# Kernel tuning notes

Hardware: AMD Instinct MI355X
Metric: run time of the kernel (lower is better)

Reference implementation:

```python
import jax, jax.numpy as jnp
import numpy as np

N = 10000
E = 320000


def setup_inputs() -> dict:
    key = jax.random.key(0)
    ks = jax.random.split(key, 10)
    return {
        "x": jax.random.normal(ks[0], (N, 384), dtype=jnp.float32),
        "edge_index": jax.random.randint(ks[1], (2, E), 0, N, dtype=jnp.int64)
        if jax.config.jax_enable_x64 else jax.random.randint(ks[1], (2, E), 0, N, dtype=jnp.int32),
        "W1": jax.random.normal(ks[2], (256, 384), dtype=jnp.float32) * 0.05,
        "b1": jax.random.normal(ks[3], (256,), dtype=jnp.float32) * 0.05,
        "W2": jax.random.normal(ks[4], (128, 256), dtype=jnp.float32) * 0.05,
        "b2": jax.random.normal(ks[5], (128,), dtype=jnp.float32) * 0.05,
        "Wa1": jax.random.normal(ks[6], (64, 128), dtype=jnp.float32) * 0.05,
        "ba1": jax.random.normal(ks[7], (64,), dtype=jnp.float32) * 0.05,
        "Wa2": jax.random.normal(ks[8], (1, 64), dtype=jnp.float32) * 0.05,
        "ba2": jax.random.normal(ks[9], (1,), dtype=jnp.float32) * 0.05,
    }


def reference(x, edge_index, W1, b1, W2, b2, Wa1, ba1, Wa2, ba2):
    # fc1 + ReLU (dropout is identity in eval mode)
    h = jax.nn.relu(x @ W1.T + b1)  # (N, hidden)
    src, tgt = edge_index[0], edge_index[1]
    n = x.shape[0]
    # bincount(target, minlength=N) -> in-degree per node (constant across the 2 passes)
    deg = jax.ops.segment_sum(jnp.ones_like(tgt, dtype=h.dtype), tgt, num_segments=n)  # (N,)
    inv = 1.0 / (deg + 1.0)  # (N,)
    for _ in range(2):
        # gather neighbor features and scatter-add into target rows
        agg = jax.ops.segment_sum(h[src], tgt, num_segments=n)  # (N, hidden)
        h = 0.7 * h + 0.3 * agg * inv[:, None]
    out = jax.nn.relu(h @ W2.T + b2)  # (N, output_dim)
    # attention MLP: Linear -> ReLU -> Linear -> Sigmoid
    att = jax.nn.sigmoid(jax.nn.relu(out @ Wa1.T + ba1) @ Wa2.T + ba2)  # (N, 1)
    return out, att
```

## Files before the change

### kernel.cpp

```cpp
#include <hip/hip_runtime.h>
#include <hip/hip_bf16.h>
#include <math.h>

#define N_NODES 10000
#define E_EDGES 320000
#define F_IN    384
#define H1      256
#define H2      128
#define ATT1    64
#define DSTRIDE 128

typedef __attribute__((ext_vector_type(8))) short bf16x8;
typedef __attribute__((ext_vector_type(4))) float f32x4;

static __device__ inline unsigned short f2bf(float f) {
    unsigned u = __float_as_uint(f);
    unsigned r = (u + 0x7fffu + ((u >> 16) & 1u)) >> 16;
    return (unsigned short)r;
}

static __device__ inline unsigned pk2bf(float a, float b) {
    __hip_bfloat162 h2 = __float22bfloat162_rn(make_float2(a, b));
    return *reinterpret_cast<unsigned*>(&h2);
}

static __device__ inline float bflo(unsigned v) { return __uint_as_float(v << 16); }
static __device__ inline float bfhi(unsigned v) { return __uint_as_float(v & 0xffff0000u); }
static __device__ inline float bf2f(short s) {
    return __uint_as_float(((unsigned)(unsigned short)s) << 16);
}

#define NW1 (H1 * F_IN / 8)
#define NW2 (H2 * H1 / 8)
#define NWA (ATT1 * H2 / 4)
#define NCZ (N_NODES / 4)
__global__ void k_conv(const float* __restrict__ W1, const float* __restrict__ W2,
                       const float* __restrict__ Wa1,
                       unsigned short* __restrict__ w1b, unsigned short* __restrict__ w2b,
                       unsigned short* __restrict__ wa1b,
                       int* __restrict__ cursor) {
    int i = blockIdx.x * blockDim.x + threadIdx.x;
    if (i < NW1) {
        int s = i;
        int jb = s / 768, rem = s - jb * 768;
        int kk = rem >> 6, lane = rem & 63;
        int ml = lane & 15, quad = lane >> 4;
        const float* p = W1 + (size_t)(jb * 16 + ml) * F_IN + kk * 32 + quad * 8;
        float4 u0 = *(const float4*)p;
        float4 u1 = *(const float4*)(p + 4);
        uint4 o;
        o.x = pk2bf(u0.x, u0.y); o.y = pk2bf(u0.z, u0.w);
        o.z = pk2bf(u1.x, u1.y); o.w = pk2bf(u1.z, u1.w);
        ((uint4*)w1b)[s] = o;
    } else if (i < NW1 + NW2) {
        int s = i - NW1;
        int jcol = s / 512, rem = s - jcol * 512;
        int kk = rem >> 6, lane = rem & 63;
        int ml = lane & 15, quad = lane >> 4;
        const float* p = W2 + (size_t)(jcol * 16 + ml) * H1 + kk * 32 + quad * 8;
        float4 u0 = *(const float4*)p;
        float4 u1 = *(const float4*)(p + 4);
        uint4 o;
        o.x = pk2bf(u0.x, u0.y); o.y = pk2bf(u0.z, u0.w);
        o.z = pk2bf(u1.x, u1.y); o.w = pk2bf(u1.z, u1.w);
        ((uint4*)w2b)[s] = o;
    } else if (i < NW1 + NW2 + NWA) {
        int j = i - NW1 - NW2;
        float4 v = ((const float4*)Wa1)[j];
        ushort4 o;
        o.x = f2bf(v.x); o.y = f2bf(v.y); o.z = f2bf(v.z); o.w = f2bf(v.w);
        ((ushort4*)wa1b)[j] = o;
    } else {
        int j = i - NW1 - NW2 - NWA;
        if (j < NCZ) ((int4*)cursor)[j] = make_int4(0, 0, 0, 0);
    }
}

#define NBLK_FC  313
#define NBLK_FIL ((E_EDGES + 1023) / 1024)
#define XS 392
#define S1 264
__global__ __launch_bounds__(256) void k_fc12fill(const float* __restrict__ x,
                                                  const unsigned short* __restrict__ w1b,
                                                  const float* __restrict__ b1,
                                                  const unsigned short* __restrict__ w2b,
                                                  unsigned short* __restrict__ z,
                                                  const int* __restrict__ srcv,
                                                  const int* __restrict__ tgt,
                                                  int* __restrict__ cursor,
                                                  int* __restrict__ csrf) {
    __shared__ unsigned short smem[32 * XS];
    if (blockIdx.x >= NBLK_FC) {
        int e0 = (blockIdx.x - NBLK_FC) * 1024 + threadIdx.x;
        #pragma unroll
        for (int q = 0; q < 4; q++) {
            int e = e0 + q * 256;
            if (e < E_EDGES) {
                int t = tgt[e];
                int p = atomicAdd(&cursor[t], 1);
                if (p < DSTRIDE)
                    __builtin_nontemporal_store(srcv[e], &csrf[t * DSTRIDE + p]);
            }
        }
        return;
    }
    int wave = threadIdx.x >> 6;
    int lane = threadIdx.x & 63;
    int m0 = blockIdx.x * 32;
    int rows = N_NODES - m0; if (rows > 32) rows = 32;
    int ml = lane & 15, quad = lane >> 4;
    {
        const float4* xsrc = (const float4*)(x + (size_t)m0 * F_IN);
        #pragma unroll
        for (int r = 0; r < 12; r++) {
            int idx = r * 256 + threadIdx.x;
            int row = idx / 96, c4 = idx - row * 96;
            unsigned* sp = (unsigned*)(smem + row * XS + c4 * 4);
            if (row < rows) {
                float4 v = xsrc[idx];
                sp[0] = pk2bf(v.x, v.y);
                sp[1] = pk2bf(v.z, v.w);
            } else {
                sp[0] = 0u; sp[1] = 0u;
            }
        }
    }
    __syncthreads();
    f32x4 acc0[4] = {{0,0,0,0},{0,0,0,0},{0,0,0,0},{0,0,0,0}};
    f32x4 acc1[4] = {{0,0,0,0},{0,0,0,0},{0,0,0,0},{0,0,0,0}};
    {
        const unsigned short* ax0 = smem + ml * XS + quad * 8;
        const unsigned short* ax1 = smem + (16 + ml) * XS + quad * 8;
        const bf16x8* W1f = (const bf16x8*)w1b;
        for (int kk = 0; kk < F_IN / 32; kk++) {
            bf16x8 a0 = *(const bf16x8*)(ax0 + kk * 32);
            bf16x8 a1 = *(const bf16x8*)(ax1 + kk * 32);
            #pragma unroll
            for (int j = 0; j < 4; j++) {
                int jb = wave * 4 + j;
                bf16x8 b = W1f[(jb * 12 + kk) * 64 + lane];
                acc0[j] = __builtin_amdgcn_mfma_f32_16x16x32_bf16(a0, b, acc0[j], 0, 0, 0);
                acc1[j] = __builtin_amdgcn_mfma_f32_16x16x32_bf16(a1, b, acc1[j], 0, 0, 0);
            }
        }
    }
    __syncthreads();
    #pragma unroll
    for (int j = 0; j < 4; j++) {
        int col = wave * 64 + j * 16 + ml;
        float bb = b1[col];
        #pragma unroll
        for (int r = 0; r < 4; r++) {
            int lr = quad * 4 + r;
            float v0 = acc0[j][r] + bb;
            float v1 = acc1[j][r] + bb;
            smem[lr * S1 + col] = f2bf(v0 > 0.f ? v0 : 0.f);
            smem[(16 + lr) * S1 + col] = f2bf(v1 > 0.f ? v1 : 0.f);
        }
    }
    __syncthreads();
    {
        int c0 = wave * 32;
        const unsigned short* pA0 = smem + ml * S1 + quad * 8;
        const unsigned short* pA1 = smem + (16 + ml) * S1 + quad * 8;
        const bf16x8* W2f = (const bf16x8*)w2b;
        f32x4 za00 = {0,0,0,0}, za01 = {0,0,0,0}, za10 = {0,0,0,0}, za11 = {0,0,0,0};
        #pragma unroll
        for (int kk = 0; kk < H1 / 32; kk++) {
            bf16x8 a0 = *(const bf16x8*)(pA0 + kk * 32);
            bf16x8 a1 = *(const bf16x8*)(pA1 + kk * 32);
            bf16x8 b0 = W2f[((wave * 2 + 0) * 8 + kk) * 64 + lane];
            bf16x8 b1v = W2f[((wave * 2 + 1) * 8 + kk) * 64 + lane];
            za00 = __builtin_amdgcn_mfma_f32_16x16x32_bf16(a0, b0, za00, 0, 0, 0);
            za01 = __builtin_amdgcn_mfma_f32_16x16x32_bf16(a0, b1v, za01, 0, 0, 0);
            za10 = __builtin_amdgcn_mfma_f32_16x16x32_bf16(a1, b0, za10, 0, 0, 0);
            za11 = __builtin_amdgcn_mfma_f32_16x16x32_bf16(a1, b1v, za11, 0, 0, 0);
        }
        #pragma unroll
        for (int r = 0; r < 4; r++) {
            int row0 = m0 + quad * 4 + r;
            z[(size_t)row0 * H2 + c0 + ml] = f2bf(za00[r]);
            z[(size_t)row0 * H2 + c0 + 16 + ml] = f2bf(za01[r]);
            int row1 = row0 + 16;
            if (row1 < N_NODES) {
                z[(size_t)row1 * H2 + c0 + ml] = f2bf(za10[r]);
                z[(size_t)row1 * H2 + c0 + 16 + ml] = f2bf(za11[r]);
            }
        }
    }
}

#define ACC8(v) { s0 += bflo(v.x); s1 += bfhi(v.x); s2 += bflo(v.y); s3 += bfhi(v.y); \
                  s4 += bflo(v.z); s5 += bfhi(v.z); s6 += bflo(v.w); s7 += bfhi(v.w); }

__global__ __launch_bounds__(256) void k_agg1(const unsigned short* __restrict__ zin,
                                              unsigned short* __restrict__ zout,
                                              const int* __restrict__ cursor,
                                              const int* __restrict__ csrf) {
    int t = blockIdx.x * 4 + (threadIdx.x >> 6);
    int lane = threadIdx.x & 63;
    int l = lane & 15, quad = lane >> 4;
    int dg = cursor[t];
    if (dg > DSTRIDE) dg = DSTRIDE;
    const uint4* base = (const uint4*)zin;
    uint4 sv = make_uint4(0, 0, 0, 0);
    if (quad == 0) sv = base[(size_t)t * 16 + l];
    float s0=0.f,s1=0.f,s2=0.f,s3=0.f,s4=0.f,s5=0.f,s6=0.f,s7=0.f;
    for (int e0 = 0; e0 < dg; e0 += 64) {
        int cnt = dg - e0; if (cnt > 64) cnt = 64;
        int c = (e0 + lane < dg) ? csrf[t * DSTRIDE + e0 + lane] : 0;
        for (int j = 0; j < cnt; j += 16) {
            int sA = __shfl(c, j + quad, 64);
            int sB = __shfl(c, j + 4 + quad, 64);
            int sC = __shfl(c, j + 8 + quad, 64);
            int sD = __shfl(c, j + 12 + quad, 64);
            uint4 vA = base[(size_t)sA * 16 + l];
            uint4 vB = base[(size_t)sB * 16 + l];
            uint4 vC = base[(size_t)sC * 16 + l];
            uint4 vD = base[(size_t)sD * 16 + l];
            if (j + quad < cnt)      ACC8(vA);
            if (j + 4 + quad < cnt)  ACC8(vB);
            if (j + 8 + quad < cnt)  ACC8(vC);
            if (j + 12 + quad < cnt) ACC8(vD);
        }
    }
    s0 += __shfl_xor(s0, 16, 64); s0 += __shfl_xor(s0, 32, 64);
    s1 += __shfl_xor(s1, 16, 64); s1 += __shfl_xor(s1, 32, 64);
    s2 += __shfl_xor(s2, 16, 64); s2 += __shfl_xor(s2, 32, 64);
    s3 += __shfl_xor(s3, 16, 64); s3 += __shfl_xor(s3, 32, 64);
    s4 += __shfl_xor(s4, 16, 64); s4 += __shfl_xor(s4, 32, 64);
    s5 += __shfl_xor(s5, 16, 64); s5 += __shfl_xor(s5, 32, 64);
    s6 += __shfl_xor(s6, 16, 64); s6 += __shfl_xor(s6, 32, 64);
    s7 += __shfl_xor(s7, 16, 64); s7 += __shfl_xor(s7, 32, 64);
    if (quad == 0) {
        float iv = 0.3f / (float)(dg + 1);
        uint4 o;
        o.x = pk2bf(0.7f * bflo(sv.x) + iv * s0, 0.7f * bfhi(sv.x) + iv * s1);
        o.y = pk2bf(0.7f * bflo(sv.y) + iv * s2, 0.7f * bfhi(sv.y) + iv * s3);
        o.z = pk2bf(0.7f * bflo(sv.z) + iv * s4, 0.7f * bfhi(sv.z) + iv * s5);
        o.w = pk2bf(0.7f * bflo(sv.w) + iv * s6, 0.7f * bfhi(sv.w) + iv * s7);
        ((uint4*)zout)[(size_t)t * 16 + l] = o;
    }
}

__global__ __launch_bounds__(256) void k_agg2fin(const unsigned short* __restrict__ zin,
                                                 const int* __restrict__ cursor,
                                                 const int* __restrict__ csrf,
                                                 const float* __restrict__ b2,
                                                 const unsigned short* __restrict__ wa1b,
                                                 const float* __restrict__ ba1,
                                                 const float* __restrict__ Wa2,
                                                 const float* __restrict__ ba2,
                                                 float* __restrict__ out,
                                                 float* __restrict__ att) {
    __shared__ float sout[4][128];
    int nl = threadIdx.x >> 6;
    int t = blockIdx.x * 4 + nl;
    int lane = threadIdx.x & 63;
    int l = lane & 15, quad = lane >> 4;
    int dg = cursor[t];
    if (dg > DSTRIDE) dg = DSTRIDE;
    const uint4* base = (const uint4*)zin;
    uint4 sv = base[(size_t)t * 16 + l];
    float s0=0.f,s1=0.f,s2=0.f,s3=0.f,s4=0.f,s5=0.f,s6=0.f,s7=0.f;
    for (int e0 = 0; e0 < dg; e0 += 64) {
        int cnt = dg - e0; if (cnt > 64) cnt = 64;
        int c = (e0 + lane < dg) ? csrf[t * DSTRIDE + e0 + lane] : 0;
        for (int j = 0; j < cnt; j += 16) {
            int sA = __shfl(c, j + quad, 64);
            int sB = __shfl(c, j + 4 + quad, 64);
            int sC = __shfl(c, j + 8 + quad, 64);
            int sD = __shfl(c, j + 12 + quad, 64);
            uint4 vA = base[(size_t)sA * 16 + l];
            uint4 vB = base[(size_t)sB * 16 + l];
            uint4 vC = base[(size_t)sC * 16 + l];
            uint4 vD = base[(size_t)sD * 16 + l];
            if (j + quad < cnt)      ACC8(vA);
            if (j + 4 + quad < cnt)  ACC8(vB);
            if (j + 8 + quad < cnt)  ACC8(vC);
            if (j + 12 + quad < cnt) ACC8(vD);
        }
    }
    s0 += __shfl_xor(s0, 16, 64); s0 += __shfl_xor(s0, 32, 64);
    s1 += __shfl_xor(s1, 16, 64); s1 += __shfl_xor(s1, 32, 64);
    s2 += __shfl_xor(s2, 16, 64); s2 += __shfl_xor(s2, 32, 64);
    s3 += __shfl_xor(s3, 16, 64); s3 += __shfl_xor(s3, 32, 64);
    s4 += __shfl_xor(s4, 16, 64); s4 += __shfl_xor(s4, 32, 64);
    s5 += __shfl_xor(s5, 16, 64); s5 += __shfl_xor(s5, 32, 64);
    s6 += __shfl_xor(s6, 16, 64); s6 += __shfl_xor(s6, 32, 64);
    s7 += __shfl_xor(s7, 16, 64); s7 += __shfl_xor(s7, 32, 64);
    float iv = 0.3f / (float)(dg + 1);
    const float4* bp = (const float4*)(b2 + l * 8);
    float4 bA = bp[0], bB = bp[1];
    float f0 = 0.7f * bflo(sv.x) + iv * s0 + bA.x;  f0 = f0 > 0.f ? f0 : 0.f;
    float f1 = 0.7f * bfhi(sv.x) + iv * s1 + bA.y;  f1 = f1 > 0.f ? f1 : 0.f;
    float f2 = 0.7f * bflo(sv.y) + iv * s2 + bA.z;  f2 = f2 > 0.f ? f2 : 0.f;
    float f3 = 0.7f * bfhi(sv.y) + iv * s3 + bA.w;  f3 = f3 > 0.f ? f3 : 0.f;
    float f4 = 0.7f * bflo(sv.z) + iv * s4 + bB.x;  f4 = f4 > 0.f ? f4 : 0.f;
    float f5 = 0.7f * bfhi(sv.z) + iv * s5 + bB.y;  f5 = f5 > 0.f ? f5 : 0.f;
    float f6 = 0.7f * bflo(sv.w) + iv * s6 + bB.z;  f6 = f6 > 0.f ? f6 : 0.f;
    float f7 = 0.7f * bfhi(sv.w) + iv * s7 + bB.w;  f7 = f7 > 0.f ? f7 : 0.f;
    float* orow = out + (size_t)t * H2 + l * 8;
    if (quad == 0) *(float4*)orow = make_float4(f0, f1, f2, f3);
    else if (quad == 1) *(float4*)(orow + 4) = make_float4(f4, f5, f6, f7);
    else if (quad == 2) *(float4*)(&sout[nl][l * 8]) = make_float4(f0, f1, f2, f3);
    else *(float4*)(&sout[nl][l * 8 + 4]) = make_float4(f4, f5, f6, f7);
    float acc = ba1[lane];
    const bf16x8* wrow = (const bf16x8*)(wa1b + (size_t)lane * H2);
    const float* srow = sout[nl];
    #pragma unroll
    for (int k8 = 0; k8 < 16; k8++) {
        bf16x8 w = wrow[k8];
        #pragma unroll
        for (int u = 0; u < 8; u++)
            acc += bf2f(w[u]) * srow[k8 * 8 + u];
    }
    float g = (acc > 0.f ? acc : 0.f) * Wa2[lane];
    #pragma unroll
    for (int d = 1; d < 64; d <<= 1) g += __shfl_xor(g, d, 64);
    if (lane == 0) att[t] = 1.f / (1.f + expf(-g));
}

extern "C" void kernel_launch(void* const* d_in, const int* in_sizes, int n_in,
                              void* d_out, int out_size, void* d_ws, size_t ws_size,
                              hipStream_t stream) {
    const float* x   = (const float*)d_in[0];
    const int*   ei  = (const int*)d_in[1];
    const float* W1  = (const float*)d_in[2];
    const float* b1  = (const float*)d_in[3];
    const float* W2  = (const float*)d_in[4];
    const float* b2  = (const float*)d_in[5];
    const float* Wa1 = (const float*)d_in[6];
    const float* ba1 = (const float*)d_in[7];
    const float* Wa2 = (const float*)d_in[8];
    const float* ba2 = (const float*)d_in[9];
    const int* srcv = ei;
    const int* tgt  = ei + E_EDGES;

    float* out_mat = (float*)d_out;
    float* att     = out_mat + N_NODES * H2;

    unsigned short* w1b  = (unsigned short*)d_ws;
    unsigned short* w2b  = w1b + (size_t)H1 * F_IN;
    unsigned short* wa1b = w2b + (size_t)H2 * H1;
    unsigned short* z0   = wa1b + (size_t)ATT1 * H2;
    unsigned short* z1   = z0 + (size_t)N_NODES * H2;
    int* cursor = (int*)(z1 + (size_t)N_NODES * H2);
    int* csrf   = cursor + N_NODES;

    {
        int total = NW1 + NW2 + NWA + NCZ;
        k_conv<<<(total + 255) / 256, 256, 0, stream>>>(W1, W2, Wa1, w1b, w2b, wa1b, cursor);
    }

    k_fc12fill<<<NBLK_FC + NBLK_FIL, 256, 0, stream>>>(x, w1b, b1, w2b, z0,
                                                       srcv, tgt, cursor, csrf);

    k_agg1<<<N_NODES / 4, 256, 0, stream>>>(z0, z1, cursor, csrf);

    k_agg2fin<<<N_NODES / 4, 256, 0, stream>>>(z1, cursor, csrf, b2,
                                               wa1b, ba1, Wa2, ba2, out_mat, att);
}
```

Before: 144.5 us.

## Unroll gather loop, read fp32 Wa1 directly, add missing ba2, plain csr stores

```diff
diff --git a/kernel.cpp b/kernel.cpp
--- a/kernel.cpp
+++ b/kernel.cpp
@@ -26,18 +26,12 @@
 
 static __device__ inline float bflo(unsigned v) { return __uint_as_float(v << 16); }
 static __device__ inline float bfhi(unsigned v) { return __uint_as_float(v & 0xffff0000u); }
-static __device__ inline float bf2f(short s) {
-    return __uint_as_float(((unsigned)(unsigned short)s) << 16);
-}
 
 #define NW1 (H1 * F_IN / 8)
 #define NW2 (H2 * H1 / 8)
-#define NWA (ATT1 * H2 / 4)
 #define NCZ (N_NODES / 4)
 __global__ void k_conv(const float* __restrict__ W1, const float* __restrict__ W2,
-                       const float* __restrict__ Wa1,
                        unsigned short* __restrict__ w1b, unsigned short* __restrict__ w2b,
-                       unsigned short* __restrict__ wa1b,
                        int* __restrict__ cursor) {
     int i = blockIdx.x * blockDim.x + threadIdx.x;
     if (i < NW1) {
@@ -64,14 +58,8 @@
         o.x = pk2bf(u0.x, u0.y); o.y = pk2bf(u0.z, u0.w);
         o.z = pk2bf(u1.x, u1.y); o.w = pk2bf(u1.z, u1.w);
         ((uint4*)w2b)[s] = o;
-    } else if (i < NW1 + NW2 + NWA) {
+    } else {
         int j = i - NW1 - NW2;
-        float4 v = ((const float4*)Wa1)[j];
-        ushort4 o;
-        o.x = f2bf(v.x); o.y = f2bf(v.y); o.z = f2bf(v.z); o.w = f2bf(v.w);
-        ((ushort4*)wa1b)[j] = o;
-    } else {
-        int j = i - NW1 - NW2 - NWA;
         if (j < NCZ) ((int4*)cursor)[j] = make_int4(0, 0, 0, 0);
     }
 }
@@ -98,8 +86,7 @@
             if (e < E_EDGES) {
                 int t = tgt[e];
                 int p = atomicAdd(&cursor[t], 1);
-                if (p < DSTRIDE)
-                    __builtin_nontemporal_store(srcv[e], &csrf[t * DSTRIDE + p]);
+                if (p < DSTRIDE) csrf[t * DSTRIDE + p] = srcv[e];
             }
         }
         return;
@@ -193,6 +180,37 @@
 #define ACC8(v) { s0 += bflo(v.x); s1 += bfhi(v.x); s2 += bflo(v.y); s3 += bfhi(v.y); \
                   s4 += bflo(v.z); s5 += bfhi(v.z); s6 += bflo(v.w); s7 += bfhi(v.w); }
 
+#define GATHER64()                                                          \
+    for (int e0 = 0; e0 < dg; e0 += 64) {                                   \
+        int cnt = dg - e0; if (cnt > 64) cnt = 64;                          \
+        int c = (e0 + lane < dg) ? csrf[t * DSTRIDE + e0 + lane] : 0;       \
+        _Pragma("unroll")                                                   \
+        for (int j = 0; j < 64; j += 16) {                                  \
+            int sA = __shfl(c, j + quad, 64);                               \
+            int sB = __shfl(c, j + 4 + quad, 64);                           \
+            int sC = __shfl(c, j + 8 + quad, 64);                           \
+            int sD = __shfl(c, j + 12 + quad, 64);                          \
+            uint4 vA = base[(size_t)sA * 16 + l];                           \
+            uint4 vB = base[(size_t)sB * 16 + l];                           \
+            uint4 vC = base[(size_t)sC * 16 + l];                           \
+            uint4 vD = base[(size_t)sD * 16 + l];                           \
+            if (j + quad < cnt)      ACC8(vA);                              \
+            if (j + 4 + quad < cnt)  ACC8(vB);                              \
+            if (j + 8 + quad < cnt)  ACC8(vC);                              \
+            if (j + 12 + quad < cnt) ACC8(vD);                              \
+        }                                                                   \
+    }
+
+#define QUADRED()                                                           \
+    s0 += __shfl_xor(s0, 16, 64); s0 += __shfl_xor(s0, 32, 64);             \
+    s1 += __shfl_xor(s1, 16, 64); s1 += __shfl_xor(s1, 32, 64);             \
+    s2 += __shfl_xor(s2, 16, 64); s2 += __shfl_xor(s2, 32, 64);             \
+    s3 += __shfl_xor(s3, 16, 64); s3 += __shfl_xor(s3, 32, 64);             \
+    s4 += __shfl_xor(s4, 16, 64); s4 += __shfl_xor(s4, 32, 64);             \
+    s5 += __shfl_xor(s5, 16, 64); s5 += __shfl_xor(s5, 32, 64);             \
+    s6 += __shfl_xor(s6, 16, 64); s6 += __shfl_xor(s6, 32, 64);             \
+    s7 += __shfl_xor(s7, 16, 64); s7 += __shfl_xor(s7, 32, 64);
+
 __global__ __launch_bounds__(256) void k_agg1(const unsigned short* __restrict__ zin,
                                               unsigned short* __restrict__ zout,
                                               const int* __restrict__ cursor,
@@ -206,32 +224,8 @@
     uint4 sv = make_uint4(0, 0, 0, 0);
     if (quad == 0) sv = base[(size_t)t * 16 + l];
     float s0=0.f,s1=0.f,s2=0.f,s3=0.f,s4=0.f,s5=0.f,s6=0.f,s7=0.f;
-    for (int e0 = 0; e0 < dg; e0 += 64) {
-        int cnt = dg - e0; if (cnt > 64) cnt = 64;
-        int c = (e0 + lane < dg) ? csrf[t * DSTRIDE + e0 + lane] : 0;
-        for (int j = 0; j < cnt; j += 16) {
-            int sA = __shfl(c, j + quad, 64);
-            int sB = __shfl(c, j + 4 + quad, 64);
-            int sC = __shfl(c, j + 8 + quad, 64);
-            int sD = __shfl(c, j + 12 + quad, 64);
-            uint4 vA = base[(size_t)sA * 16 + l];
-            uint4 vB = base[(size_t)sB * 16 + l];
-            uint4 vC = base[(size_t)sC * 16 + l];
-            uint4 vD = base[(size_t)sD * 16 + l];
-            if (j + quad < cnt)      ACC8(vA);
-            if (j + 4 + quad < cnt)  ACC8(vB);
-            if (j + 8 + quad < cnt)  ACC8(vC);
-            if (j + 12 + quad < cnt) ACC8(vD);
-        }
-    }
-    s0 += __shfl_xor(s0, 16, 64); s0 += __shfl_xor(s0, 32, 64);
-    s1 += __shfl_xor(s1, 16, 64); s1 += __shfl_xor(s1, 32, 64);
-    s2 += __shfl_xor(s2, 16, 64); s2 += __shfl_xor(s2, 32, 64);
-    s3 += __shfl_xor(s3, 16, 64); s3 += __shfl_xor(s3, 32, 64);
-    s4 += __shfl_xor(s4, 16, 64); s4 += __shfl_xor(s4, 32, 64);
-    s5 += __shfl_xor(s5, 16, 64); s5 += __shfl_xor(s5, 32, 64);
-    s6 += __shfl_xor(s6, 16, 64); s6 += __shfl_xor(s6, 32, 64);
-    s7 += __shfl_xor(s7, 16, 64); s7 += __shfl_xor(s7, 32, 64);
+    GATHER64();
+    QUADRED();
     if (quad == 0) {
         float iv = 0.3f / (float)(dg + 1);
         uint4 o;
@@ -247,7 +241,7 @@
                                                  const int* __restrict__ cursor,
                                                  const int* __restrict__ csrf,
                                                  const float* __restrict__ b2,
-                                                 const unsigned short* __restrict__ wa1b,
+                                                 const float* __restrict__ Wa1,
                                                  const float* __restrict__ ba1,
                                                  const float* __restrict__ Wa2,
                                                  const float* __restrict__ ba2,
@@ -263,32 +257,8 @@
     const uint4* base = (const uint4*)zin;
     uint4 sv = base[(size_t)t * 16 + l];
     float s0=0.f,s1=0.f,s2=0.f,s3=0.f,s4=0.f,s5=0.f,s6=0.f,s7=0.f;
-    for (int e0 = 0; e0 < dg; e0 += 64) {
-        int cnt = dg - e0; if (cnt > 64) cnt = 64;
-        int c = (e0 + lane < dg) ? csrf[t * DSTRIDE + e0 + lane] : 0;
-        for (int j = 0; j < cnt; j += 16) {
-            int sA = __shfl(c, j + quad, 64);
-            int sB = __shfl(c, j + 4 + quad, 64);
-            int sC = __shfl(c, j + 8 + quad, 64);
-            int sD = __shfl(c, j + 12 + quad, 64);
-            uint4 vA = base[(size_t)sA * 16 + l];
-            uint4 vB = base[(size_t)sB * 16 + l];
-            uint4 vC = base[(size_t)sC * 16 + l];
-            uint4 vD = base[(size_t)sD * 16 + l];
-            if (j + quad < cnt)      ACC8(vA);
-            if (j + 4 + quad < cnt)  ACC8(vB);
-            if (j + 8 + quad < cnt)  ACC8(vC);
-            if (j + 12 + quad < cnt) ACC8(vD);
-        }
-    }
-    s0 += __shfl_xor(s0, 16, 64); s0 += __shfl_xor(s0, 32, 64);
-    s1 += __shfl_xor(s1, 16, 64); s1 += __shfl_xor(s1, 32, 64);
-    s2 += __shfl_xor(s2, 16, 64); s2 += __shfl_xor(s2, 32, 64);
-    s3 += __shfl_xor(s3, 16, 64); s3 += __shfl_xor(s3, 32, 64);
-    s4 += __shfl_xor(s4, 16, 64); s4 += __shfl_xor(s4, 32, 64);
-    s5 += __shfl_xor(s5, 16, 64); s5 += __shfl_xor(s5, 32, 64);
-    s6 += __shfl_xor(s6, 16, 64); s6 += __shfl_xor(s6, 32, 64);
-    s7 += __shfl_xor(s7, 16, 64); s7 += __shfl_xor(s7, 32, 64);
+    GATHER64();
+    QUADRED();
     float iv = 0.3f / (float)(dg + 1);
     const float4* bp = (const float4*)(b2 + l * 8);
     float4 bA = bp[0], bB = bp[1];
@@ -306,19 +276,18 @@
     else if (quad == 2) *(float4*)(&sout[nl][l * 8]) = make_float4(f0, f1, f2, f3);
     else *(float4*)(&sout[nl][l * 8 + 4]) = make_float4(f4, f5, f6, f7);
     float acc = ba1[lane];
-    const bf16x8* wrow = (const bf16x8*)(wa1b + (size_t)lane * H2);
+    const float4* wrow = (const float4*)(Wa1 + (size_t)lane * H2);
     const float* srow = sout[nl];
     #pragma unroll
-    for (int k8 = 0; k8 < 16; k8++) {
-        bf16x8 w = wrow[k8];
-        #pragma unroll
-        for (int u = 0; u < 8; u++)
-            acc += bf2f(w[u]) * srow[k8 * 8 + u];
+    for (int k4 = 0; k4 < 32; k4++) {
+        float4 w = wrow[k4];
+        acc += w.x * srow[k4 * 4 + 0] + w.y * srow[k4 * 4 + 1]
+             + w.z * srow[k4 * 4 + 2] + w.w * srow[k4 * 4 + 3];
     }
     float g = (acc > 0.f ? acc : 0.f) * Wa2[lane];
     #pragma unroll
     for (int d = 1; d < 64; d <<= 1) g += __shfl_xor(g, d, 64);
-    if (lane == 0) att[t] = 1.f / (1.f + expf(-g));
+    if (lane == 0) att[t] = 1.f / (1.f + expf(-(g + ba2[0])));
 }
 
 extern "C" void kernel_launch(void* const* d_in, const int* in_sizes, int n_in,
@@ -340,17 +309,16 @@
     float* out_mat = (float*)d_out;
     float* att     = out_mat + N_NODES * H2;
 
-    unsigned short* w1b  = (unsigned short*)d_ws;
-    unsigned short* w2b  = w1b + (size_t)H1 * F_IN;
-    unsigned short* wa1b = w2b + (size_t)H2 * H1;
-    unsigned short* z0   = wa1b + (size_t)ATT1 * H2;
-    unsigned short* z1   = z0 + (size_t)N_NODES * H2;
+    unsigned short* w1b = (unsigned short*)d_ws;
+    unsigned short* w2b = w1b + (size_t)H1 * F_IN;
+    unsigned short* z0  = w2b + (size_t)H2 * H1;
+    unsigned short* z1  = z0 + (size_t)N_NODES * H2;
     int* cursor = (int*)(z1 + (size_t)N_NODES * H2);
     int* csrf   = cursor + N_NODES;
 
     {
-        int total = NW1 + NW2 + NWA + NCZ;
-        k_conv<<<(total + 255) / 256, 256, 0, stream>>>(W1, W2, Wa1, w1b, w2b, wa1b, cursor);
+        int total = NW1 + NW2 + NCZ;
+        k_conv<<<(total + 255) / 256, 256, 0, stream>>>(W1, W2, w1b, w2b, cursor);
     }
 
     k_fc12fill<<<NBLK_FC + NBLK_FIL, 256, 0, stream>>>(x, w1b, b1, w2b, z0,
@@ -359,5 +327,5 @@
     k_agg1<<<N_NODES / 4, 256, 0, stream>>>(z0, z1, cursor, csrf);
 
     k_agg2fin<<<N_NODES / 4, 256, 0, stream>>>(z1, cursor, csrf, b2,
-                                               wa1b, ba1, Wa2, ba2, out_mat, att);
-}
+                                               Wa1, ba1, Wa2, ba2, out_mat, att);
+}
```

Measured after the change: 162.6 us. 1.13x slower.
